# Kernel optimization log

Hardware: AMD Instinct MI355X
Metric: run time of the kernel (lower is better)

## Reference

```python
import jax, jax.numpy as jnp
import numpy as np

N = 50000        # nodes
E = 800000       # edges
F_IN = 64
HID = [128, 256, 256]
G = 512          # graphs in batch
C = 6            # classes
EPS = 1e-5


def setup_inputs() -> dict:
    key = jax.random.key(0)
    ks = jax.random.split(key, 32)
    inp = {}
    inp['x'] = jax.random.normal(ks[0], (N, F_IN), dtype=jnp.float32)
    inp['edge_index'] = jax.random.randint(ks[1], (2, E), 0, N, dtype=jnp.int64)
    inp['batch'] = jnp.sort(jax.random.randint(ks[2], (N,), 0, G, dtype=jnp.int64))
    dims = [F_IN] + HID
    i = 3
    for l in range(3):
        d_in, d_out = dims[l], dims[l + 1]
        inp[f'W{l+1}'] = jax.random.normal(ks[i], (d_in, d_out), dtype=jnp.float32) * (1.0 / np.sqrt(d_in)); i += 1
        inp[f'b{l+1}'] = jnp.zeros((d_out,), dtype=jnp.float32)
        inp[f'g{l+1}'] = jnp.ones((d_out,), dtype=jnp.float32)
        inp[f'be{l+1}'] = jnp.zeros((d_out,), dtype=jnp.float32)
        inp[f'm{l+1}'] = jax.random.normal(ks[i], (d_out,), dtype=jnp.float32) * 0.1; i += 1
        inp[f'v{l+1}'] = jax.random.uniform(ks[i], (d_out,), dtype=jnp.float32, minval=0.5, maxval=1.5); i += 1
    mlp_dims = [(2 * HID[-1], 256), (256, 128), (128, C)]
    for l, (d_in, d_out) in enumerate(mlp_dims):
        inp[f'Wm{l+1}'] = jax.random.normal(ks[i], (d_in, d_out), dtype=jnp.float32) * (1.0 / np.sqrt(d_in)); i += 1
        inp[f'bm{l+1}'] = jnp.zeros((d_out,), dtype=jnp.float32)
    return inp


def _forward(x, edge_index, batch,
             W1, b1, g1, be1, m1, v1,
             W2, b2, g2, be2, m2, v2,
             W3, b3, g3, be3, m3, v3,
             Wm1, bm1, Wm2, bm2, Wm3, bm3):
    src, dst = edge_index[0], edge_index[1]
    loops = jnp.arange(N, dtype=src.dtype)
    src_sl = jnp.concatenate([src, loops])   # self-loops, as in PyG GCNConv
    dst_sl = jnp.concatenate([dst, loops])
    deg = jax.ops.segment_sum(jnp.ones_like(src_sl, dtype=x.dtype), dst_sl, num_segments=N)
    dis = jnp.where(deg > 0, jax.lax.rsqrt(deg), 0.0)
    norm = dis[src_sl] * dis[dst_sl]          # [E+N]

    def gcn(h, W, b):
        h = h @ W                              # transform first (PyG order)
        msg = h[src_sl] * norm[:, None]        # gather + scale
        return jax.ops.segment_sum(msg, dst_sl, num_segments=N) + b

    def bn_relu(h, g, be, m, v):
        return jax.nn.relu((h - m) * jax.lax.rsqrt(v + EPS) * g + be)

    h = bn_relu(gcn(x, W1, b1), g1, be1, m1, v1)
    h = bn_relu(gcn(h, W2, b2), g2, be2, m2, v2)
    h = bn_relu(gcn(h, W3, b3), g3, be3, m3, v3)

    counts = jax.ops.segment_sum(jnp.ones((N,), dtype=h.dtype), batch, num_segments=G)
    x_mean = jax.ops.segment_sum(h, batch, num_segments=G) / jnp.maximum(counts, 1.0)[:, None]
    x_max = jax.ops.segment_max(h, batch, num_segments=G)
    x_max = jnp.where(counts[:, None] > 0, x_max, 0.0)
    z = jnp.concatenate([x_mean, x_max], axis=1)   # [G, 512]

    z = jax.nn.gelu(z @ Wm1 + bm1, approximate=False)
    z = jax.nn.gelu(z @ Wm2 + bm2, approximate=False)
    return z @ Wm3 + bm3                            # [G, C]


def reference(x, edge_index, batch,
              W1, b1, g1, be1, m1, v1,
              W2, b2, g2, be2, m2, v2,
              W3, b3, g3, be3, m3, v3,
              Wm1, bm1, Wm2, bm2, Wm3, bm3):
    return _forward(x, edge_index, batch,
                    W1, b1, g1, be1, m1, v1,
                    W2, b2, g2, be2, m2, v2,
                    W3, b3, g3, be3, m3, v3,
                    Wm1, bm1, Wm2, bm2, Wm3, bm3)
```

## Files before the change

### kernel.cpp

```cpp
#include <hip/hip_runtime.h>
#include <hip/hip_bf16.h>
#include <hip/hip_fp16.h>

typedef __hip_bfloat16 bf16;
typedef unsigned short u16;
typedef short bfrag __attribute__((ext_vector_type(8)));
typedef float f32x4 __attribute__((ext_vector_type(4)));
typedef unsigned u32x2 __attribute__((ext_vector_type(2)));

#define NGRAPH 512
#define BN_EPS 1e-5f
#define NBUCK 64

__device__ __forceinline__ float b2f(bf16 x) { return __bfloat162float(x); }
__device__ __forceinline__ float bf_lo(unsigned u) { return __uint_as_float(u << 16); }
__device__ __forceinline__ float bf_hi(unsigned u) { return __uint_as_float(u & 0xffff0000u); }
__device__ __forceinline__ u16 f2u(float v) {
    bf16 t = __float2bfloat16(v);
    u16 r; __builtin_memcpy(&r, &t, 2); return r;
}

__device__ __forceinline__ float load_f(const void* p, int i, int isbf16) {
    if (isbf16) {
        unsigned short u = ((const unsigned short*)p)[i];
        return __uint_as_float(((unsigned int)u) << 16);
    }
    return ((const float*)p)[i];
}

__global__ void detect_dtype(const void* __restrict__ x, int* __restrict__ flag) {
    int lane = threadIdx.x & 63;
    unsigned short u = ((const unsigned short*)x)[2 * lane];
    float f = __uint_as_float(((unsigned int)u) << 16);
    int crazy = (!(fabsf(f) <= 1024.0f)) ? 1 : 0;
    unsigned long long m = __ballot(crazy);
    if (threadIdx.x == 0) *flag = (m == 0ULL) ? 1 : 0;
}

__global__ void cvt_bf_s(const void* __restrict__ in, u16* __restrict__ out,
                         int n, int npad, const int* __restrict__ flag) {
    int i = blockIdx.x * blockDim.x + threadIdx.x;
    if (i >= n * 64) return;
    int node = i >> 6, f = i & 63;
    out[((size_t)(f >> 5) * npad + node) * 32 + (f & 31)] = f2u(load_f(in, i, *flag));
}

__global__ void repack_w(const void* __restrict__ W, u16* __restrict__ out,
                         int Kd, int Nd, const int* __restrict__ flag) {
    int t = blockIdx.x * blockDim.x + threadIdx.x;
    if (t >= Kd * Nd) return;
    int isbf = *flag;
    int j = t & 7;
    int lane = (t >> 3) & 63;
    int tile = t >> 9;
    int NT = Nd / 16;
    int nt = tile % NT, kt = tile / NT;
    int k = kt * 32 + (lane >> 4) * 8 + j;
    int nn = nt * 16 + (lane & 15);
    out[t] = f2u(load_f(W, k * Nd + nn, isbf));
}

__device__ __forceinline__ void fold_one(const void* b, const void* g, const void* be,
                                         const void* m, const void* v,
                                         float* S, float* T, int f, int isbf) {
    float bb = load_f(b, f, isbf), gg = load_f(g, f, isbf);
    float bee = load_f(be, f, isbf), mm = load_f(m, f, isbf);
    float vv = load_f(v, f, isbf);
    float s = gg * rsqrtf(vv + BN_EPS);
    S[f] = s;
    T[f] = (bb - mm) * s + bee;
}

__global__ void fold_bn_all(
    const void* b1, const void* g1, const void* be1, const void* m1, const void* v1,
    const void* b2, const void* g2, const void* be2, const void* m2, const void* v2,
    const void* b3, const void* g3, const void* be3, const void* m3, const void* v3,
    float* S1, float* T1, float* S2, float* T2, float* S3, float* T3,
    const int* __restrict__ flag) {
    int t = blockIdx.x * blockDim.x + threadIdx.x;
    int isbf = *flag;
    if (t < 128) fold_one(b1, g1, be1, m1, v1, S1, T1, t, isbf);
    else if (t < 384) fold_one(b2, g2, be2, m2, v2, S2, T2, t - 128, isbf);
    else if (t < 640) fold_one(b3, g3, be3, m3, v3, S3, T3, t - 384, isbf);
}

__global__ void init_csr(int* __restrict__ deg, int* __restrict__ total,
                         int* __restrict__ bcnt, int n) {
    int i = blockIdx.x * blockDim.x + threadIdx.x;
    if (i < n) deg[i] = 0;
    if (i < NBUCK) bcnt[i] = 0;
    if (i == 0) *total = 0;
}

__global__ void count_deg_i(const int* __restrict__ dst, int* __restrict__ deg, int e) {
    int i = blockIdx.x * blockDim.x + threadIdx.x;
    if (i < e) atomicAdd(&deg[dst[i]], 1);
}

__global__ void reserve_rows(const int* __restrict__ deg, int* __restrict__ row_start,
                             int* __restrict__ cursor, float* __restrict__ dis,
                             unsigned* __restrict__ csrw,
                             int* __restrict__ total, int* __restrict__ bcnt, int n) {
    __shared__ int lh[NBUCK];
    int tid = threadIdx.x;
    if (tid < NBUCK) lh[tid] = 0;
    __syncthreads();
    int i = blockIdx.x * blockDim.x + tid;
    if (i < n) {
        int d = deg[i];
        int dpad = (d + 7) & ~7;
        int s = atomicAdd(total, dpad);
        row_start[i] = s;
        cursor[i] = s;
        dis[i] = rsqrtf((float)(d + 1));
        atomicAdd(&lh[min(d, NBUCK - 1)], 1);
        unsigned val = (unsigned)(i & 0xffff);
        for (int k = d; k < dpad; k++) csrw[s + k] = val;
    }
    __syncthreads();
    if (tid < NBUCK) {
        int c = lh[tid];
        if (c) atomicAdd(&bcnt[tid], c);
    }
}

__global__ void bucket_prefix(const int* __restrict__ bcnt, int* __restrict__ bcur) {
    if (threadIdx.x == 0 && blockIdx.x == 0) {
        int acc = 0;
        for (int i = 0; i < NBUCK; i++) { bcur[i] = acc; acc += bcnt[i]; }
    }
}

__global__ void bucket_scatter(const int* __restrict__ deg, const int* __restrict__ rowst,
                               int* __restrict__ bcur, uint4* __restrict__ ninfo, int n) {
    __shared__ int lh[NBUCK];
    __shared__ int lbase[NBUCK];
    int tid = threadIdx.x;
    if (tid < NBUCK) lh[tid] = 0;
    __syncthreads();
    int i = blockIdx.x * blockDim.x + tid;
    int b = 0, lr = 0;
    if (i < n) {
        b = min(deg[i], NBUCK - 1);
        lr = atomicAdd(&lh[b], 1);
    }
    __syncthreads();
    if (tid < NBUCK) {
        int c = lh[tid];
        lbase[tid] = c ? atomicAdd(&bcur[tid], c) : 0;
    }
    __syncthreads();
    if (i < n) ninfo[lbase[b] + lr] = make_uint4(i, rowst[i], deg[i], 0);
}

__global__ void scatter_edges(const int* __restrict__ src, const int* __restrict__ dst,
                              const float* __restrict__ dis, int* __restrict__ cursor,
                              unsigned* __restrict__ csrw, int e) {
    int i = blockIdx.x * blockDim.x + threadIdx.x;
    if (i >= e) return;
    int s = src[i], dt = dst[i];
    int pos = atomicAdd(&cursor[dt], 1);
    float nw = dis[s] * dis[dt];
    unsigned short h = __half_as_ushort(__float2half(nw));
    csrw[pos] = (unsigned)(s & 0xffff) | ((unsigned)h << 16);
}

template <int NSLICE>
__global__ __launch_bounds__(256) void csr_agg_s5(
    const uint4* __restrict__ ninfo, const unsigned* __restrict__ csrw,
    const u16* __restrict__ hs, u16* __restrict__ AG, int n, int npad) {
    constexpr int F = NSLICE * 32;
    int slice = blockIdx.x % NSLICE;
    int nb = blockIdx.x / NSLICE;
    int lane = threadIdx.x & 63;
    int wv = threadIdx.x >> 6;
    int sub = lane >> 3, ls = lane & 7;
    int oidx = nb * 32 + wv * 8 + sub;
    if (oidx >= n) return;
    uint4 nf = ninfo[oidx];
    int node = (int)nf.x;
    int start = (int)nf.y;
    int d = (int)nf.z;
    int dpad = (d + 7) & ~7;
    float dd = 1.0f / (float)(d + 1);
    const u16* __restrict__ base = hs + (size_t)slice * npad * 32;

    float a0, a1, a2, a3;
    {
        uint2 u = *(const uint2*)(base + (size_t)node * 32 + ls * 4);
        a0 = bf_lo(u.x) * dd; a1 = bf_hi(u.x) * dd;
        a2 = bf_lo(u.y) * dd; a3 = bf_hi(u.y) * dd;
    }

    const unsigned* __restrict__ ep = csrw + start;
    unsigned mc[8];
    if (dpad) {
#pragma unroll
        for (int j = 0; j < 8; j++) mc[j] = ep[j];
    }
    for (int k = 0; k < dpad; k += 8) {
        unsigned mn[8];
        if (k + 8 < dpad) {
#pragma unroll
            for (int j = 0; j < 8; j++) mn[j] = ep[k + 8 + j];
        }
        float w[8];
        uint2 q[8];
#pragma unroll
        for (int j = 0; j < 8; j++) {
            int s = (int)(mc[j] & 0xffffu);
            w[j] = __half2float(__ushort_as_half((unsigned short)(mc[j] >> 16)));
            q[j] = *(const uint2*)(base + (size_t)s * 32 + ls * 4);
        }
#pragma unroll
        for (int j = 0; j < 8; j++) {
            a0 += w[j] * bf_lo(q[j].x); a1 += w[j] * bf_hi(q[j].x);
            a2 += w[j] * bf_lo(q[j].y); a3 += w[j] * bf_hi(q[j].y);
        }
#pragma unroll
        for (int j = 0; j < 8; j++) mc[j] = mn[j];
    }
    u32x2 o;
    o.x = (unsigned)f2u(a0) | ((unsigned)f2u(a1) << 16);
    o.y = (unsigned)f2u(a2) | ((unsigned)f2u(a3) << 16);
    __builtin_nontemporal_store(o, (u32x2*)(AG + (size_t)node * F + slice * 32 + ls * 4));
}

template <int K, int N, int NSLICE_OUT>
__global__ __launch_bounds__(256) void mfma_gemm_bn(
    const u16* __restrict__ A, const u16* __restrict__ Wrep,
    const float* __restrict__ S, const float* __restrict__ T,
    u16* __restrict__ C, int M, int npad) {
    constexpr int KP = K + 8;
    constexpr int NT = N / 16;
    constexpr int KT = K / 32;
    __shared__ u16 Alds[64 * KP];
    const int m0 = blockIdx.x * 64;
    const int tid = threadIdx.x;
    for (int c = tid; c < 64 * (K / 8); c += 256) {
        int r = c / (K / 8), kc = c % (K / 8);
        uint4 v = *(const uint4*)(A + (size_t)(m0 + r) * K + kc * 8);
        *(uint4*)(&Alds[r * KP + kc * 8]) = v;
    }
    __syncthreads();
    const int wv = tid >> 6, lane = tid & 63;
    const int mrow = lane & 15;
    const int kb = lane >> 4;
    f32x4 acc[NT];
#pragma unroll
    for (int nt = 0; nt < NT; nt++) acc[nt] = (f32x4){0.f, 0.f, 0.f, 0.f};
#pragma unroll
    for (int kt = 0; kt < KT; kt++) {
        bfrag a = *(const bfrag*)(&Alds[(wv * 16 + mrow) * KP + kt * 32 + kb * 8]);
#pragma unroll
        for (int nt = 0; nt < NT; nt++) {
            bfrag b = *(const bfrag*)(Wrep + ((size_t)(kt * NT + nt) * 64 + lane) * 8);
            acc[nt] = __builtin_amdgcn_mfma_f32_16x16x32_bf16(a, b, acc[nt], 0, 0, 0);
        }
    }
#pragma unroll
    for (int nt = 0; nt < NT; nt++) {
        int f = nt * 16 + mrow;
        float s = S[f];
        float t = T[f];
#pragma unroll
        for (int r = 0; r < 4; r++) {
            int row = m0 + wv * 16 + kb * 4 + r;
            if (row < M) {
                u16 val = f2u(fmaxf(acc[nt][r] * s + t, 0.0f));
                if (NSLICE_OUT > 0)
                    C[((size_t)(f >> 5) * npad + row) * 32 + (f & 31)] = val;
                else
                    C[(size_t)row * N + f] = val;
            }
        }
    }
}

__global__ void init_pool(float* __restrict__ psum, float* __restrict__ pmax,
                          int* __restrict__ pcnt) {
    int i = blockIdx.x * blockDim.x + threadIdx.x;
    if (i < NGRAPH * 256) { psum[i] = 0.f; pmax[i] = 0.f; }
    if (i < NGRAPH) pcnt[i] = 0;
}

#define POOL_NC 64
__global__ __launch_bounds__(256) void pool_seg(
    const u16* __restrict__ h, const int* __restrict__ batch,
    float* __restrict__ psum, float* __restrict__ pmax,
    int* __restrict__ pcnt, int n) {
    int wid = (int)(((size_t)blockIdx.x * blockDim.x + threadIdx.x) >> 6);
    int lane = threadIdx.x & 63;
    int n0 = wid * POOL_NC;
    if (n0 >= n) return;
    int n1 = min(n0 + POOL_NC, n);

    float sum[4] = {0.f, 0.f, 0.f, 0.f};
    float mx[4] = {0.f, 0.f, 0.f, 0.f};
    int cnt = 0;
    int gcur = batch[n0];

    uint2 u_next = *(const uint2*)(h + (size_t)n0 * 256 + lane * 4);
    int g_next = gcur;

    for (int node = n0; node < n1; node++) {
        uint2 u = u_next;
        int g = g_next;
        if (node + 1 < n1) {
            u_next = *(const uint2*)(h + (size_t)(node + 1) * 256 + lane * 4);
            g_next = batch[node + 1];
        }
        if (g != gcur) {
#pragma unroll
            for (int c = 0; c < 4; c++) {
                atomicAdd(&psum[gcur * 256 + lane * 4 + c], sum[c]);
                atomicMax((int*)&pmax[gcur * 256 + lane * 4 + c], __float_as_int(mx[c]));
                sum[c] = 0.f; mx[c] = 0.f;
            }
            if (lane == 0) atomicAdd(&pcnt[gcur], cnt);
            cnt = 0;
            gcur = g;
        }
        float v0 = bf_lo(u.x), v1 = bf_hi(u.x), v2 = bf_lo(u.y), v3 = bf_hi(u.y);
        sum[0] += v0; sum[1] += v1; sum[2] += v2; sum[3] += v3;
        mx[0] = fmaxf(mx[0], v0); mx[1] = fmaxf(mx[1], v1);
        mx[2] = fmaxf(mx[2], v2); mx[3] = fmaxf(mx[3], v3);
        cnt++;
    }
#pragma unroll
    for (int c = 0; c < 4; c++) {
        atomicAdd(&psum[gcur * 256 + lane * 4 + c], sum[c]);
        atomicMax((int*)&pmax[gcur * 256 + lane * 4 + c], __float_as_int(mx[c]));
    }
    if (lane == 0) atomicAdd(&pcnt[gcur], cnt);
}

__global__ void build_z(const float* __restrict__ psum, const float* __restrict__ pmax,
                        const int* __restrict__ pcnt, float* __restrict__ z) {
    int i = blockIdx.x * blockDim.x + threadIdx.x;
    if (i >= NGRAPH * 256) return;
    int g = i >> 8, f = i & 255;
    float c = (float)max(pcnt[g], 1);
    z[g * 512 + f] = psum[i] / c;
    z[g * 512 + 256 + f] = pmax[i];
}

template <int K, int NOUT, bool GELU>
__global__ void mlp_gemm(const float* __restrict__ A, const void* __restrict__ W,
                         const void* __restrict__ bias, float* __restrict__ C,
                         const int* __restrict__ flag) {
    __shared__ float a[K];
    int row = blockIdx.x;
    for (int idx = threadIdx.x; idx < K; idx += blockDim.x) a[idx] = A[row * K + idx];
    __syncthreads();
    int col = threadIdx.x;
    if (col < NOUT) {
        int isbf = *flag;
        float acc = load_f(bias, col, isbf);
        if (isbf) {
            const bf16* w = (const bf16*)W;
            for (int k = 0; k < K; k++) acc += a[k] * b2f(w[k * NOUT + col]);
        } else {
            const float* w = (const float*)W;
            for (int k = 0; k < K; k++) acc += a[k] * w[k * NOUT + col];
        }
        if (GELU) acc = 0.5f * acc * (1.0f + erff(acc * 0.70710678118654752f));
        C[row * NOUT + col] = acc;
    }
}

__global__ void write_out(const float* __restrict__ in, void* __restrict__ out,
                          int n, const int* __restrict__ flag) {
    int i = blockIdx.x * blockDim.x + threadIdx.x;
    if (i >= n) return;
    if (*flag) ((bf16*)out)[i] = __float2bfloat16(in[i]);
    else       ((float*)out)[i] = in[i];
}

extern "C" void kernel_launch(void* const* d_in, const int* in_sizes, int n_in,
                              void* d_out, int out_size, void* d_ws, size_t ws_size,
                              hipStream_t stream) {
    const void* x     = d_in[0];
    const int*  ei    = (const int*)d_in[1];
    const int*  batch = (const int*)d_in[2];
    const void *W1 = d_in[3],  *b1 = d_in[4],  *g1 = d_in[5],  *be1 = d_in[6],  *m1 = d_in[7],  *v1 = d_in[8];
    const void *W2 = d_in[9],  *b2 = d_in[10], *g2 = d_in[11], *be2 = d_in[12], *m2 = d_in[13], *v2 = d_in[14];
    const void *W3 = d_in[15], *b3 = d_in[16], *g3 = d_in[17], *be3 = d_in[18], *m3 = d_in[19], *v3 = d_in[20];
    const void *Wm1 = d_in[21], *bm1 = d_in[22];
    const void *Wm2 = d_in[23], *bm2 = d_in[24];
    const void *Wm3 = d_in[25], *bm3 = d_in[26];

    const int n = in_sizes[0] / 64;
    const int E = in_sizes[1] / 2;
    const int* src = ei;
    const int* dst = ei + E;
    const int npad = (n + 63 + 64) & ~63;

    size_t off = 0;
    auto carve = [&](size_t bytes) {
        void* p = (char*)d_ws + off;
        off += (bytes + 255) & ~(size_t)255;
        return p;
    };
    int*      flag  = (int*)carve(4);
    int*      total = (int*)carve(4);
    int*      bcnt  = (int*)carve(NBUCK * 4);
    int*      bcur  = (int*)carve(NBUCK * 4);
    float*    dis   = (float*)carve((size_t)n * 4);
    int*      deg_i = (int*)carve((size_t)n * 4);
    int*      rowst = (int*)carve((size_t)n * 4);
    int*      curs  = (int*)carve((size_t)n * 4);
    uint4*    ninfo = (uint4*)carve((size_t)n * 16);
    unsigned* csrw  = (unsigned*)carve(((size_t)E + 8 * (size_t)n) * 4);
    u16*      xs    = (u16*)carve((size_t)npad * 64 * 2);
    u16*      Hs    = (u16*)carve((size_t)npad * 256 * 2);
    u16*      AG    = (u16*)carve((size_t)npad * 256 * 2);
    u16*      H     = (u16*)carve((size_t)npad * 256 * 2);
    u16*      W1r   = (u16*)carve((size_t)64 * 128 * 2);
    u16*      W2r   = (u16*)carve((size_t)128 * 256 * 2);
    u16*      W3r   = (u16*)carve((size_t)256 * 256 * 2);
    float* S1 = (float*)carve(128 * 4); float* T1 = (float*)carve(128 * 4);
    float* S2 = (float*)carve(256 * 4); float* T2 = (float*)carve(256 * 4);
    float* S3 = (float*)carve(256 * 4); float* T3 = (float*)carve(256 * 4);
    float* psum = (float*)carve((size_t)NGRAPH * 256 * 4);
    float* pmax = (float*)carve((size_t)NGRAPH * 256 * 4);
    int*   pcnt = (int*)carve((size_t)NGRAPH * 4);
    float* z    = (float*)carve((size_t)NGRAPH * 512 * 4);
    float* z1   = (float*)carve((size_t)NGRAPH * 256 * 4);
    float* z2   = (float*)carve((size_t)NGRAPH * 128 * 4);
    float* z3   = (float*)carve((size_t)NGRAPH * 8 * 4);
    (void)ws_size; (void)n_in;

    const int BT = 256;

    detect_dtype<<<1, 64, 0, stream>>>(x, flag);
    cvt_bf_s<<<(n * 64 + BT - 1) / BT, BT, 0, stream>>>(x, xs, n, npad, flag);
    repack_w<<<(64 * 128 + BT - 1) / BT, BT, 0, stream>>>(W1, W1r, 64, 128, flag);
    repack_w<<<(128 * 256 + BT - 1) / BT, BT, 0, stream>>>(W2, W2r, 128, 256, flag);
    repack_w<<<(256 * 256 + BT - 1) / BT, BT, 0, stream>>>(W3, W3r, 256, 256, flag);
    fold_bn_all<<<3, 256, 0, stream>>>(b1, g1, be1, m1, v1, b2, g2, be2, m2, v2,
                                       b3, g3, be3, m3, v3, S1, T1, S2, T2, S3, T3, flag);

    init_csr<<<(n + BT - 1) / BT, BT, 0, stream>>>(deg_i, total, bcnt, n);
    count_deg_i<<<(E + BT - 1) / BT, BT, 0, stream>>>(dst, deg_i, E);
    reserve_rows<<<(n + BT - 1) / BT, BT, 0, stream>>>(deg_i, rowst, curs, dis, csrw, total, bcnt, n);
    bucket_prefix<<<1, 64, 0, stream>>>(bcnt, bcur);
    bucket_scatter<<<(n + BT - 1) / BT, BT, 0, stream>>>(deg_i, rowst, bcur, ninfo, n);
    scatter_edges<<<(E + BT - 1) / BT, BT, 0, stream>>>(src, dst, dis, curs, csrw, E);

    const int gblocks = (n + 63) / 64;
    const int nb32 = (n + 31) / 32;

    csr_agg_s5<2><<<2 * nb32, 256, 0, stream>>>(ninfo, csrw, xs, AG, n, npad);
    mfma_gemm_bn<64, 128, 4><<<gblocks, 256, 0, stream>>>(AG, W1r, S1, T1, Hs, n, npad);

    csr_agg_s5<4><<<4 * nb32, 256, 0, stream>>>(ninfo, csrw, Hs, AG, n, npad);
    mfma_gemm_bn<128, 256, 8><<<gblocks, 256, 0, stream>>>(AG, W2r, S2, T2, Hs, n, npad);

    csr_agg_s5<8><<<8 * nb32, 256, 0, stream>>>(ninfo, csrw, Hs, AG, n, npad);
    mfma_gemm_bn<256, 256, 0><<<gblocks, 256, 0, stream>>>(AG, W3r, S3, T3, H, n, npad);

    init_pool<<<(NGRAPH * 256 + BT - 1) / BT, BT, 0, stream>>>(psum, pmax, pcnt);
    const int pool_waves = (n + POOL_NC - 1) / POOL_NC;
    pool_seg<<<(pool_waves * 64 + BT - 1) / BT, BT, 0, stream>>>(H, batch, psum, pmax, pcnt, n);
    build_z<<<(NGRAPH * 256 + BT - 1) / BT, BT, 0, stream>>>(psum, pmax, pcnt, z);

    mlp_gemm<512, 256, true><<<NGRAPH, 256, 0, stream>>>(z, Wm1, bm1, z1, flag);
    mlp_gemm<256, 128, true><<<NGRAPH, 256, 0, stream>>>(z1, Wm2, bm2, z2, flag);
    mlp_gemm<128, 6, false><<<NGRAPH, 128, 0, stream>>>(z2, Wm3, bm3, z3, flag);
    write_out<<<(NGRAPH * 6 + BT - 1) / BT, BT, 0, stream>>>(z3, d_out, NGRAPH * 6, flag);
}
```

Before: 476.0 us.

## Split GEMM output columns across blocks and keep weight fragments in registers

```diff
diff --git a/kernel.cpp b/kernel.cpp
--- a/kernel.cpp
+++ b/kernel.cpp
@@ -226,48 +226,60 @@
     __builtin_nontemporal_store(o, (u32x2*)(AG + (size_t)node * F + slice * 32 + ls * 4));
 }
 
-template <int K, int N, int NSLICE_OUT>
-__global__ __launch_bounds__(256) void mfma_gemm_bn(
+template <int K, int N, int NSUB, int NSLICE_OUT>
+__global__ __launch_bounds__(256) void mfma_gemm_rb(
     const u16* __restrict__ A, const u16* __restrict__ Wrep,
     const float* __restrict__ S, const float* __restrict__ T,
     u16* __restrict__ C, int M, int npad) {
     constexpr int KP = K + 8;
     constexpr int NT = N / 16;
     constexpr int KT = K / 32;
+    constexpr int NSPLIT = NT / NSUB;
     __shared__ u16 Alds[64 * KP];
-    const int m0 = blockIdx.x * 64;
+    const int mt = blockIdx.x / NSPLIT;
+    const int ns = blockIdx.x - mt * NSPLIT;
+    const int m0 = mt * 64;
     const int tid = threadIdx.x;
+    const int lane = tid & 63;
+    const int wv = tid >> 6;
+
+    bfrag breg[KT * NSUB];
+#pragma unroll
+    for (int kt = 0; kt < KT; kt++)
+#pragma unroll
+        for (int j = 0; j < NSUB; j++)
+            breg[kt * NSUB + j] = *(const bfrag*)(Wrep +
+                ((size_t)(kt * NT + ns * NSUB + j) * 64 + lane) * 8);
+
     for (int c = tid; c < 64 * (K / 8); c += 256) {
         int r = c / (K / 8), kc = c % (K / 8);
         uint4 v = *(const uint4*)(A + (size_t)(m0 + r) * K + kc * 8);
         *(uint4*)(&Alds[r * KP + kc * 8]) = v;
     }
     __syncthreads();
-    const int wv = tid >> 6, lane = tid & 63;
+
     const int mrow = lane & 15;
     const int kb = lane >> 4;
-    f32x4 acc[NT];
-#pragma unroll
-    for (int nt = 0; nt < NT; nt++) acc[nt] = (f32x4){0.f, 0.f, 0.f, 0.f};
+    f32x4 acc[NSUB];
+#pragma unroll
+    for (int j = 0; j < NSUB; j++) acc[j] = (f32x4){0.f, 0.f, 0.f, 0.f};
 #pragma unroll
     for (int kt = 0; kt < KT; kt++) {
         bfrag a = *(const bfrag*)(&Alds[(wv * 16 + mrow) * KP + kt * 32 + kb * 8]);
 #pragma unroll
-        for (int nt = 0; nt < NT; nt++) {
-            bfrag b = *(const bfrag*)(Wrep + ((size_t)(kt * NT + nt) * 64 + lane) * 8);
-            acc[nt] = __builtin_amdgcn_mfma_f32_16x16x32_bf16(a, b, acc[nt], 0, 0, 0);
-        }
-    }
-#pragma unroll
-    for (int nt = 0; nt < NT; nt++) {
-        int f = nt * 16 + mrow;
+        for (int j = 0; j < NSUB; j++)
+            acc[j] = __builtin_amdgcn_mfma_f32_16x16x32_bf16(a, breg[kt * NSUB + j], acc[j], 0, 0, 0);
+    }
+#pragma unroll
+    for (int j = 0; j < NSUB; j++) {
+        int f = (ns * NSUB + j) * 16 + mrow;
         float s = S[f];
         float t = T[f];
 #pragma unroll
         for (int r = 0; r < 4; r++) {
             int row = m0 + wv * 16 + kb * 4 + r;
             if (row < M) {
-                u16 val = f2u(fmaxf(acc[nt][r] * s + t, 0.0f));
+                u16 val = f2u(fmaxf(acc[j][r] * s + t, 0.0f));
                 if (NSLICE_OUT > 0)
                     C[((size_t)(f >> 5) * npad + row) * 32 + (f & 31)] = val;
                 else
@@ -452,13 +464,13 @@
     const int nb32 = (n + 31) / 32;
 
     csr_agg_s5<2><<<2 * nb32, 256, 0, stream>>>(ninfo, csrw, xs, AG, n, npad);
-    mfma_gemm_bn<64, 128, 4><<<gblocks, 256, 0, stream>>>(AG, W1r, S1, T1, Hs, n, npad);
+    mfma_gemm_rb<64, 128, 8, 4><<<gblocks, 256, 0, stream>>>(AG, W1r, S1, T1, Hs, n, npad);
 
     csr_agg_s5<4><<<4 * nb32, 256, 0, stream>>>(ninfo, csrw, Hs, AG, n, npad);
-    mfma_gemm_bn<128, 256, 8><<<gblocks, 256, 0, stream>>>(AG, W2r, S2, T2, Hs, n, npad);
+    mfma_gemm_rb<128, 256, 4, 8><<<gblocks * 4, 256, 0, stream>>>(AG, W2r, S2, T2, Hs, n, npad);
 
     csr_agg_s5<8><<<8 * nb32, 256, 0, stream>>>(ninfo, csrw, Hs, AG, n, npad);
-    mfma_gemm_bn<256, 256, 0><<<gblocks, 256, 0, stream>>>(AG, W3r, S3, T3, H, n, npad);
+    mfma_gemm_rb<256, 256, 4, 0><<<gblocks * 4, 256, 0, stream>>>(AG, W3r, S3, T3, H, n, npad);
 
     init_pool<<<(NGRAPH * 256 + BT - 1) / BT, BT, 0, stream>>>(psum, pmax, pcnt);
     const int pool_waves = (n + POOL_NC - 1) / POOL_NC;
```

Measured after the change: 461.3 us. -3.1%, faster.
